# Kernel tuning notes

Measured on AMD Instinct MI355X. Metric: run time of the kernel, lower is better.

The kernel has to match this reference:

```python
import jax, jax.numpy as jnp
import numpy as np

N_NODES = 20000
N_EDGES = 640000
NODE_DIM = 128
EDGE_DIM = 128
HIDDEN = max(NODE_DIM, EDGE_DIM)  # 128


def _linear_init(key, fan_in, fan_out):
    # torch nn.Linear default: U(-1/sqrt(fan_in), 1/sqrt(fan_in))
    kw, kb = jax.random.split(key)
    bound = 1.0 / np.sqrt(fan_in)
    W = jax.random.uniform(kw, (fan_in, fan_out), jnp.float32, -bound, bound)
    b = jax.random.uniform(kb, (fan_out,), jnp.float32, -bound, bound)
    return W, b


def setup_inputs() -> dict:
    key = jax.random.key(0)
    ks = jax.random.split(key, 8)
    node_feat = jax.random.normal(ks[0], (N_NODES, NODE_DIM), jnp.float32)
    edge_feat = jax.random.normal(ks[1], (N_EDGES, EDGE_DIM), jnp.float32)
    edge_index = jax.random.randint(ks[2], (2, N_EDGES), 0, N_NODES, jnp.int64)
    W1e, b1e = _linear_init(ks[3], 2 * NODE_DIM + EDGE_DIM, HIDDEN)
    W2e, b2e = _linear_init(ks[4], HIDDEN, EDGE_DIM)
    W1n, b1n = _linear_init(ks[5], NODE_DIM + EDGE_DIM, NODE_DIM)
    W2n, b2n = _linear_init(ks[6], NODE_DIM, NODE_DIM)
    return {
        "node_feat": node_feat, "edge_feat": edge_feat, "edge_index": edge_index,
        "W1e": W1e, "b1e": b1e, "W2e": W2e, "b2e": b2e,
        "W1n": W1n, "b1n": b1n, "W2n": W2n, "b2n": b2n,
    }


def reference(node_feat, edge_feat, edge_index, W1e, b1e, W2e, b2e, W1n, b1n, W2n, b2n):
    src, dst = edge_index[0], edge_index[1]
    n_nodes = node_feat.shape[0]

    # Edge update: gather endpoints, concat, MLP, residual.
    edge_input = jnp.concatenate([edge_feat, node_feat[src], node_feat[dst]], axis=-1)
    h = jax.nn.silu(edge_input @ W1e + b1e)
    edge_feat = edge_feat + (h @ W2e + b2e)

    # Mean aggregation of updated edge feats into dst nodes (clamped counts).
    agg = jax.ops.segment_sum(edge_feat, dst, num_segments=n_nodes)
    counts = jax.ops.segment_sum(jnp.ones((dst.shape[0],), edge_feat.dtype), dst,
                                 num_segments=n_nodes)
    agg = agg / jnp.maximum(counts, 1.0)[:, None]

    # Node update: concat, MLP, residual.
    node_input = jnp.concatenate([node_feat, agg], axis=-1)
    g = jax.nn.silu(node_input @ W1n + b1n)
    node_feat = node_feat + (g @ W2n + b2n)
    return (node_feat, edge_feat)
```

## Files before the change

kernel.cpp:

```cpp
#include <hip/hip_runtime.h>
#include <hip/hip_bf16.h>
#include <stdint.h>

#define N_NODES 20000
#define N_EDGES 640000
#define DIM 128
#define TPB 10
#define EDGE_GRID 500

using bf16x8 = __attribute__((ext_vector_type(8))) short;
using f32x4  = __attribute__((ext_vector_type(4))) float;

static __device__ __forceinline__ unsigned short f2bf(float f) {
    union { float f; unsigned int u; } v; v.f = f;
    unsigned int r = v.u + 0x7FFFu + ((v.u >> 16) & 1u);
    return (unsigned short)(r >> 16);
}

static __device__ __forceinline__ void glds16(const unsigned short* g, char* lds) {
    __builtin_amdgcn_global_load_lds(
        (const __attribute__((address_space(1))) unsigned int*)(const void*)g,
        (__attribute__((address_space(3))) unsigned int*)(void*)lds, 16, 0, 0);
}

static __device__ __forceinline__ void lds_fence() {
    __builtin_amdgcn_sched_barrier(0);
    asm volatile("s_waitcnt lgkmcnt(0)" ::: "memory");
    __builtin_amdgcn_sched_barrier(0);
}
static __device__ __forceinline__ void ds_order() {
    __builtin_amdgcn_sched_barrier(0x7F);
}

__global__ void prep_kernel(const float* __restrict__ node_feat,
                            const float* __restrict__ W1e, const float* __restrict__ W2e,
                            const float* __restrict__ W1n, const float* __restrict__ W2n,
                            unsigned short* __restrict__ node_bf,
                            unsigned short* __restrict__ Wt1e, unsigned short* __restrict__ Wt2e,
                            unsigned short* __restrict__ Wt1n, unsigned short* __restrict__ Wt2n,
                            int* __restrict__ counts) {
    int tid = blockIdx.x * blockDim.x + threadIdx.x;
    int stride = gridDim.x * blockDim.x;
    for (int i = tid; i < N_NODES * DIM / 8; i += stride) {
        const float* p = node_feat + (size_t)i * 8;
        float4 f0 = *(const float4*)p;
        float4 f1 = *(const float4*)(p + 4);
        bf16x8 a;
        a[0] = (short)f2bf(f0.x); a[1] = (short)f2bf(f0.y);
        a[2] = (short)f2bf(f0.z); a[3] = (short)f2bf(f0.w);
        a[4] = (short)f2bf(f1.x); a[5] = (short)f2bf(f1.y);
        a[6] = (short)f2bf(f1.z); a[7] = (short)f2bf(f1.w);
        *(bf16x8*)(node_bf + (size_t)i * 8) = a;
    }
    for (int i = tid; i < DIM * 384; i += stride) { int n = i / 384, k = i % 384; Wt1e[i] = f2bf(W1e[k * DIM + n]); }
    for (int i = tid; i < DIM * DIM; i += stride) { int n = i / DIM, k = i % DIM; Wt2e[i] = f2bf(W2e[k * DIM + n]); }
    for (int i = tid; i < DIM * 256; i += stride) { int n = i / 256, k = i % 256; Wt1n[i] = f2bf(W1n[k * DIM + n]); }
    for (int i = tid; i < DIM * DIM; i += stride) { int n = i / DIM, k = i % DIM; Wt2n[i] = f2bf(W2n[k * DIM + n]); }
    for (int i = tid; i < N_NODES; i += stride) counts[i] = 0;
}

__global__ void count_kernel(const int* __restrict__ eidx, int* __restrict__ counts) {
    int e = blockIdx.x * blockDim.x + threadIdx.x;
    if (e < N_EDGES) atomicAdd(&counts[eidx[N_EDGES + e]], 1);
}

__global__ void scan_kernel(const int* __restrict__ counts, int* __restrict__ offsets,
                            int* __restrict__ cursor) {
    __shared__ int wsum[16];
    const int CH = 20;
    int tid = threadIdx.x;
    int lane = tid & 63, wid = tid >> 6;
    int base = tid * CH;
    int s = 0;
    #pragma unroll
    for (int j = 0; j < CH; ++j) { int i = base + j; s += (i < N_NODES) ? counts[i] : 0; }
    int chunk = s;
    #pragma unroll
    for (int off = 1; off < 64; off <<= 1) { int t = __shfl_up(s, off, 64); if (lane >= off) s += t; }
    if (lane == 63) wsum[wid] = s;
    __syncthreads();
    if (tid == 0) {
        int run = 0;
        for (int w = 0; w < 16; ++w) { int t = wsum[w]; wsum[w] = run; run += t; }
    }
    __syncthreads();
    int run = wsum[wid] + s - chunk;
    for (int j = 0; j < CH; ++j) {
        int i = base + j;
        if (i < N_NODES) { offsets[i] = run; cursor[i] = run; run += counts[i]; }
    }
}

__global__ void scatter_kernel(const int* __restrict__ eidx, int* __restrict__ cursor,
                               int* __restrict__ elist) {
    int e = blockIdx.x * blockDim.x + threadIdx.x;
    if (e < N_EDGES) {
        int p = atomicAdd(&cursor[eidx[N_EDGES + e]], 1);
        elist[p] = e;
    }
}

__launch_bounds__(256, 1)
__global__ void edge_kernel(const float* __restrict__ edge_feat,
                            const int* __restrict__ eidx,
                            const unsigned short* __restrict__ node_bf,
                            const unsigned short* __restrict__ Wt1e,
                            const unsigned short* __restrict__ Wt2e,
                            const float* __restrict__ b1e,
                            const float* __restrict__ b2e,
                            float* __restrict__ out_edge) {
    __shared__ char ldsW1[98304];
    __shared__ char ldsW2[32768];
    __shared__ char ldsS[4][4096];
    const int tid = threadIdx.x;
    const int wv = tid >> 6;
    const int l = tid & 63;
    const int lr = l & 15;
    const int kg = l >> 4;
    char* S = ldsS[wv];
    const int eBase = blockIdx.x * (TPB * 128);

    #pragma unroll
    for (int c = 0; c < 24; ++c) {
        int Sc = c * 256 + tid;
        int n = Sc / 48, sp = Sc % 48;
        int s = (sp & 56) | ((sp ^ n) & 7);
        glds16(Wt1e + n * 384 + s * 8, ldsW1 + Sc * 16);
    }
    #pragma unroll
    for (int c = 0; c < 8; ++c) {
        int Sc = c * 256 + tid;
        int n = Sc >> 4, sp = Sc & 15;
        int s = (sp & 8) | ((sp ^ n) & 7);
        glds16(Wt2e + n * 128 + s * 8, ldsW2 + Sc * 16);
    }

    float b1r[8], b2r[8];
    #pragma unroll
    for (int tt = 0; tt < 8; ++tt) { b1r[tt] = b1e[tt * 16 + lr]; b2r[tt] = b2e[tt * 16 + lr]; }

    float4 E0[4][2][2], E1[4][2][2];
    bf16x8 N0[8][2], N1[8][2];

    auto prefRaw = [&](int t, float4 (&E)[4][2][2], bf16x8 (&NB)[8][2]) {
        int tb = eBase + t * 128 + wv * 32;
        int e0 = tb + lr, e1 = tb + 16 + lr;
        int s0 = eidx[e0], d0 = eidx[N_EDGES + e0];
        int s1 = eidx[e1], d1 = eidx[N_EDGES + e1];
        #pragma unroll
        for (int st = 0; st < 4; ++st) {
            const float* p0 = edge_feat + (long)e0 * DIM + st * 32 + kg * 8;
            const float* p1 = edge_feat + (long)e1 * DIM + st * 32 + kg * 8;
            E[st][0][0] = *(const float4*)p0; E[st][0][1] = *(const float4*)(p0 + 4);
            E[st][1][0] = *(const float4*)p1; E[st][1][1] = *(const float4*)(p1 + 4);
        }
        #pragma unroll
        for (int st = 0; st < 4; ++st) {
            NB[st][0]     = *(const bf16x8*)(node_bf + (long)s0 * DIM + st * 32 + kg * 8);
            NB[st][1]     = *(const bf16x8*)(node_bf + (long)s1 * DIM + st * 32 + kg * 8);
            NB[st + 4][0] = *(const bf16x8*)(node_bf + (long)d0 * DIM + st * 32 + kg * 8);
            NB[st + 4][1] = *(const bf16x8*)(node_bf + (long)d1 * DIM + st * 32 + kg * 8);
        }
    };

    f32x4 acc[2][8];

    auto gemm1 = [&](float4 (&E)[4][2][2], bf16x8 (&NB)[8][2]) {
        bf16x8 EB[4][2];
        #pragma unroll
        for (int st = 0; st < 4; ++st)
            #pragma unroll
            for (int rt = 0; rt < 2; ++rt) {
                bf16x8 a;
                a[0] = (short)f2bf(E[st][rt][0].x); a[1] = (short)f2bf(E[st][rt][0].y);
                a[2] = (short)f2bf(E[st][rt][0].z); a[3] = (short)f2bf(E[st][rt][0].w);
                a[4] = (short)f2bf(E[st][rt][1].x); a[5] = (short)f2bf(E[st][rt][1].y);
                a[6] = (short)f2bf(E[st][rt][1].z); a[7] = (short)f2bf(E[st][rt][1].w);
                EB[st][rt] = a;
            }
        #pragma unroll
        for (int rt = 0; rt < 2; ++rt)
            #pragma unroll
            for (int tt = 0; tt < 8; ++tt) acc[rt][tt] = (f32x4){0.f, 0.f, 0.f, 0.f};
        #pragma unroll
        for (int s = 0; s < 12; ++s) {
            int sl = s * 4 + kg;
            int sp = (sl & 56) | ((sl ^ lr) & 7);
            #pragma unroll
            for (int tt = 0; tt < 8; ++tt) {
                bf16x8 B = *(const bf16x8*)(ldsW1 + (tt * 16 + lr) * 768 + sp * 16);
                #pragma unroll
                for (int rt = 0; rt < 2; ++rt) {
                    bf16x8 A = (s < 4) ? EB[s][rt] : NB[s - 4][rt];
                    acc[rt][tt] = __builtin_amdgcn_mfma_f32_16x16x32_bf16(A, B, acc[rt][tt], 0, 0, 0);
                }
            }
        }
    };

    auto tail = [&](int t) {
        int tb = eBase + t * 128 + wv * 32;
        f32x4 acc2[2][8];
        #pragma unroll
        for (int rt = 0; rt < 2; ++rt)
            #pragma unroll
            for (int tt = 0; tt < 8; ++tt) acc2[rt][tt] = (f32x4){0.f, 0.f, 0.f, 0.f};

        #pragma unroll
        for (int q = 0; q < 4; ++q) {
            #pragma unroll
            for (int rt = 0; rt < 2; ++rt)
                #pragma unroll
                for (int t2 = 0; t2 < 2; ++t2) {
                    int tt = q * 2 + t2;
                    #pragma unroll
                    for (int r = 0; r < 4; ++r) {
                        int row = rt * 16 + kg * 4 + r;
                        float x = acc[rt][tt][r] + b1r[tt];
                        float h = x / (1.0f + __expf(-x));
                        int slot = t2 * 2 + (lr >> 3);
                        int byte = row * 64 + ((slot ^ ((row >> 1) & 3)) << 4) + (lr & 7) * 2;
                        *(unsigned short*)(S + byte) = f2bf(h);
                    }
                }
            lds_fence();
            bf16x8 A2[2];
            #pragma unroll
            for (int rt = 0; rt < 2; ++rt) {
                int row = rt * 16 + lr;
                int byte = row * 64 + ((kg ^ ((row >> 1) & 3)) << 4);
                A2[rt] = *(const bf16x8*)(S + byte);
            }
            ds_order();
            int sl2 = q * 4 + kg;
            int sp2 = (sl2 & 8) | ((sl2 ^ lr) & 7);
            #pragma unroll
            for (int tt = 0; tt < 8; ++tt) {
                bf16x8 B = *(const bf16x8*)(ldsW2 + (tt * 16 + lr) * 256 + sp2 * 16);
                #pragma unroll
                for (int rt = 0; rt < 2; ++rt)
                    acc2[rt][tt] = __builtin_amdgcn_mfma_f32_16x16x32_bf16(A2[rt], B, acc2[rt][tt], 0, 0, 0);
            }
        }

        #pragma unroll
        for (int rt = 0; rt < 2; ++rt)
            #pragma unroll
            for (int ch = 0; ch < 2; ++ch) {
                #pragma unroll
                for (int t2 = 0; t2 < 4; ++t2) {
                    int tt = ch * 4 + t2;
                    #pragma unroll
                    for (int r = 0; r < 4; ++r) {
                        int row = kg * 4 + r;
                        int col = t2 * 16 + lr;
                        int byte = row * 256 + (((col >> 2) ^ (row & 15)) << 4) + (col & 3) * 4;
                        *(float*)(S + byte) = acc2[rt][tt][r] + b2r[tt];
                    }
                }
                lds_fence();
                #pragma unroll
                for (int i = 0; i < 4; ++i) {
                    int row = (l >> 4) + i * 4;
                    int slot = l & 15;
                    int byte = row * 256 + ((slot ^ (row & 15)) << 4);
                    float4 v = *(const float4*)(S + byte);
                    long gidx = (long)(tb + rt * 16 + row) * DIM + ch * 64 + slot * 4;
                    float4 rs = *(const float4*)(edge_feat + gidx);
                    v.x += rs.x; v.y += rs.y; v.z += rs.z; v.w += rs.w;
                    *(float4*)(out_edge + gidx) = v;
                }
                ds_order();
            }
    };

    prefRaw(0, E0, N0);
    __syncthreads();

    #pragma unroll 1
    for (int it = 0; it < TPB / 2; ++it) {
        int t0 = it * 2;
        prefRaw(t0 + 1, E1, N1);
        gemm1(E0, N0);
        tail(t0);
        if (t0 + 2 < TPB) prefRaw(t0 + 2, E0, N0);
        gemm1(E1, N1);
        tail(t0 + 1);
    }
}

__global__ void agg_kernel(const float* __restrict__ edge_out,
                           const int* __restrict__ offsets, const int* __restrict__ counts,
                           const int* __restrict__ elist,
                           unsigned short* __restrict__ agg_bf) {
    int n = blockIdx.x * 4 + (threadIdx.x >> 6);
    int l = threadIdx.x & 63;
    if (n >= N_NODES) return;
    int off = offsets[n], cnt = counts[n];
    float a0 = 0.f, a1 = 0.f;
    int i = 0;
    for (; i + 4 <= cnt; i += 4) {
        int e0 = elist[off + i], e1 = elist[off + i + 1];
        int e2 = elist[off + i + 2], e3 = elist[off + i + 3];
        float2 v0 = *(const float2*)(edge_out + (long)e0 * DIM + l * 2);
        float2 v1 = *(const float2*)(edge_out + (long)e1 * DIM + l * 2);
        float2 v2 = *(const float2*)(edge_out + (long)e2 * DIM + l * 2);
        float2 v3 = *(const float2*)(edge_out + (long)e3 * DIM + l * 2);
        a0 += v0.x + v1.x + v2.x + v3.x;
        a1 += v0.y + v1.y + v2.y + v3.y;
    }
    for (; i < cnt; ++i) {
        int e = elist[off + i];
        float2 v = *(const float2*)(edge_out + (long)e * DIM + l * 2);
        a0 += v.x; a1 += v.y;
    }
    float inv = 1.0f / fmaxf((float)cnt, 1.0f);
    agg_bf[n * DIM + l * 2] = f2bf(a0 * inv);
    agg_bf[n * DIM + l * 2 + 1] = f2bf(a1 * inv);
}

#define SLICE_B 8448
__launch_bounds__(256, 4)
__global__ void node_kernel(const float* __restrict__ node_feat,
                            const unsigned short* __restrict__ node_bf,
                            const unsigned short* __restrict__ agg_bf,
                            const unsigned short* __restrict__ Wt1n,
                            const unsigned short* __restrict__ Wt2n,
                            const float* __restrict__ b1n,
                            const float* __restrict__ b2n,
                            float* __restrict__ out_node) {
    __shared__ char lds[4][SLICE_B];
    const int tid = threadIdx.x;
    const int wv = tid >> 6;
    const int l = tid & 63;
    const int lr = l & 15;
    const int kg = l >> 4;
    char* slice = lds[wv];

    const int nBase = blockIdx.x * 128;
    const int wBase = nBase + wv * 32;

    int rowc[2];
    #pragma unroll
    for (int rt = 0; rt < 2; ++rt) {
        int row = wBase + rt * 16 + lr;
        rowc[rt] = row < N_NODES ? row : N_NODES - 1;
    }

    f32x4 acc[2][8];
    #pragma unroll
    for (int rt = 0; rt < 2; ++rt)
        #pragma unroll
        for (int t = 0; t < 8; ++t) acc[rt][t] = (f32x4){0.f, 0.f, 0.f, 0.f};

    #pragma unroll
    for (int s = 0; s < 8; ++s) {
        const int kk = s * 32 + kg * 8;
        bf16x8 A[2];
        if (s < 4) {
            #pragma unroll
            for (int rt = 0; rt < 2; ++rt)
                A[rt] = *(const bf16x8*)(node_bf + (long)rowc[rt] * DIM + kk);
        } else {
            #pragma unroll
            for (int rt = 0; rt < 2; ++rt)
                A[rt] = *(const bf16x8*)(agg_bf + (long)rowc[rt] * DIM + (kk - 128));
        }
        #pragma unroll
        for (int t = 0; t < 8; ++t) {
            bf16x8 B = *(const bf16x8*)(Wt1n + (t * 16 + lr) * 256 + kk);
            #pragma unroll
            for (int rt = 0; rt < 2; ++rt)
                acc[rt][t] = __builtin_amdgcn_mfma_f32_16x16x32_bf16(A[rt], B, acc[rt][t], 0, 0, 0);
        }
    }

    #pragma unroll
    for (int rt = 0; rt < 2; ++rt) {
        #pragma unroll
        for (int t = 0; t < 8; ++t) {
            float b1 = b1n[t * 16 + lr];
            int col = t * 16 + lr;
            #pragma unroll
            for (int r = 0; r < 4; ++r) {
                int row = rt * 16 + kg * 4 + r;
                float x = acc[rt][t][r] + b1;
                float h = x / (1.0f + __expf(-x));
                int byte = (row * 256 + col * 2) ^ ((row & 7) << 4);
                *(unsigned short*)(slice + byte) = f2bf(h);
            }
        }
    }
    __syncthreads();

    f32x4 acc2[2][8];
    #pragma unroll
    for (int rt = 0; rt < 2; ++rt)
        #pragma unroll
        for (int t = 0; t < 8; ++t) acc2[rt][t] = (f32x4){0.f, 0.f, 0.f, 0.f};

    #pragma unroll
    for (int s = 0; s < 4; ++s) {
        const int kk = s * 32 + kg * 8;
        bf16x8 A[2];
        #pragma unroll
        for (int rt = 0; rt < 2; ++rt) {
            int row = rt * 16 + lr;
            int byte = (row * 256 + kk * 2) ^ ((row & 7) << 4);
            A[rt] = *(const bf16x8*)(slice + byte);
        }
        #pragma unroll
        for (int t = 0; t < 8; ++t) {
            bf16x8 B = *(const bf16x8*)(Wt2n + (t * 16 + lr) * DIM + kk);
            #pragma unroll
            for (int rt = 0; rt < 2; ++rt)
                acc2[rt][t] = __builtin_amdgcn_mfma_f32_16x16x32_bf16(A[rt], B, acc2[rt][t], 0, 0, 0);
        }
    }
    __syncthreads();

    #pragma unroll
    for (int rt = 0; rt < 2; ++rt) {
        float* sf = (float*)slice;
        #pragma unroll
        for (int t = 0; t < 8; ++t) {
            float b2 = b2n[t * 16 + lr];
            int col = t * 16 + lr;
            #pragma unroll
            for (int r = 0; r < 4; ++r) {
                int row = kg * 4 + r;
                int colp = col ^ (row & 12);
                sf[row * 132 + colp] = acc2[rt][t][r] + b2;
            }
        }
        __syncthreads();
        #pragma unroll
        for (int rr = 0; rr < 8; ++rr) {
            int row = rr * 2 + (l >> 5);
            int c4 = (l & 31) * 4;
            int cswz = c4 ^ (row & 12);
            float4 v = *(const float4*)(sf + row * 132 + cswz);
            int grow = wBase + rt * 16 + row;
            if (grow < N_NODES) {
                long gidx = (long)grow * DIM + c4;
                float4 rsd = *(const float4*)(node_feat + gidx);
                v.x += rsd.x; v.y += rsd.y; v.z += rsd.z; v.w += rsd.w;
                *(float4*)(out_node + gidx) = v;
            }
        }
        __syncthreads();
    }
}

extern "C" void kernel_launch(void* const* d_in, const int* in_sizes, int n_in,
                              void* d_out, int out_size, void* d_ws, size_t ws_size,
                              hipStream_t stream) {
    const float* node_feat = (const float*)d_in[0];
    const float* edge_feat = (const float*)d_in[1];
    const int*   eidx      = (const int*)d_in[2];
    const float* W1e = (const float*)d_in[3];
    const float* b1e = (const float*)d_in[4];
    const float* W2e = (const float*)d_in[5];
    const float* b2e = (const float*)d_in[6];
    const float* W1n = (const float*)d_in[7];
    const float* b1n = (const float*)d_in[8];
    const float* W2n = (const float*)d_in[9];
    const float* b2n = (const float*)d_in[10];

    char* ws = (char*)d_ws;
    size_t off = 0;
    auto alloc = [&](size_t bytes) {
        void* p = ws + off;
        off += (bytes + 255) & ~(size_t)255;
        return p;
    };
    unsigned short* node_bf = (unsigned short*)alloc((size_t)N_NODES * DIM * 2);
    unsigned short* agg_bf  = (unsigned short*)alloc((size_t)N_NODES * DIM * 2);
    unsigned short* Wt1e    = (unsigned short*)alloc((size_t)DIM * 384 * 2);
    unsigned short* Wt2e    = (unsigned short*)alloc((size_t)DIM * DIM * 2);
    unsigned short* Wt1n    = (unsigned short*)alloc((size_t)DIM * 256 * 2);
    unsigned short* Wt2n    = (unsigned short*)alloc((size_t)DIM * DIM * 2);
    int* counts  = (int*)alloc((size_t)N_NODES * 4);
    int* offsets = (int*)alloc((size_t)N_NODES * 4);
    int* cursor  = (int*)alloc((size_t)N_NODES * 4);
    int* elist   = (int*)alloc((size_t)N_EDGES * 4);

    float* out_node = (float*)d_out;
    float* out_edge = out_node + (size_t)N_NODES * DIM;

    prep_kernel<<<512, 256, 0, stream>>>(node_feat, W1e, W2e, W1n, W2n,
                                         node_bf, Wt1e, Wt2e, Wt1n, Wt2n, counts);
    count_kernel<<<(N_EDGES + 255) / 256, 256, 0, stream>>>(eidx, counts);
    scan_kernel<<<1, 1024, 0, stream>>>(counts, offsets, cursor);
    scatter_kernel<<<(N_EDGES + 255) / 256, 256, 0, stream>>>(eidx, cursor, elist);
    edge_kernel<<<EDGE_GRID, 256, 0, stream>>>(edge_feat, eidx, node_bf, Wt1e, Wt2e,
                                               b1e, b2e, out_edge);
    agg_kernel<<<(N_NODES + 3) / 4, 256, 0, stream>>>(out_edge, offsets, counts, elist, agg_bf);
    node_kernel<<<(N_NODES + 127) / 128, 256, 0, stream>>>(node_feat, node_bf, agg_bf,
                                                           Wt1n, Wt2n, b1n, b2n, out_node);
}
```

Baseline: 518.8 us.

## Double edge-kernel block to 8 waves, single-buffer prefetch, preload residuals

The edge kernel goes from 4 to 8 waves per block (512 threads, launch bounds 512,2). Each block still covers the same 1280 edges in 5 tiles of 256. The explicit double-buffered register prefetch is replaced by a single buffer refilled after each tile, leaving latency hiding to the extra waves. Residual edge_feat rows are loaded ahead of the second GEMM, and the aggregation loop is widened to issue 8 gathers per step. This trades register-level software pipelining for more wave-level parallelism, with the risk of register-pressure spills under the new launch bounds and LDS limits on occupancy.

```diff
diff --git a/kernel.cpp b/kernel.cpp
--- a/kernel.cpp
+++ b/kernel.cpp
@@ -5,7 +5,7 @@
 #define N_NODES 20000
 #define N_EDGES 640000
 #define DIM 128
-#define TPB 10
+#define TPB 5
 #define EDGE_GRID 500
 
 using bf16x8 = __attribute__((ext_vector_type(8))) short;
@@ -30,6 +30,9 @@
 }
 static __device__ __forceinline__ void ds_order() {
     __builtin_amdgcn_sched_barrier(0x7F);
+}
+static __device__ __forceinline__ void vmem_order() {
+    __builtin_amdgcn_sched_barrier(0x38F);
 }
 
 __global__ void prep_kernel(const float* __restrict__ node_feat,
@@ -100,7 +103,7 @@
     }
 }
 
-__launch_bounds__(256, 1)
+__launch_bounds__(512, 2)
 __global__ void edge_kernel(const float* __restrict__ edge_feat,
                             const int* __restrict__ eidx,
                             const unsigned short* __restrict__ node_bf,
@@ -111,25 +114,25 @@
                             float* __restrict__ out_edge) {
     __shared__ char ldsW1[98304];
     __shared__ char ldsW2[32768];
-    __shared__ char ldsS[4][4096];
+    __shared__ char ldsS[8][4096];
     const int tid = threadIdx.x;
     const int wv = tid >> 6;
     const int l = tid & 63;
     const int lr = l & 15;
     const int kg = l >> 4;
     char* S = ldsS[wv];
-    const int eBase = blockIdx.x * (TPB * 128);
-
-    #pragma unroll
-    for (int c = 0; c < 24; ++c) {
-        int Sc = c * 256 + tid;
+    const int eBase = blockIdx.x * (TPB * 256);
+
+    #pragma unroll
+    for (int c = 0; c < 12; ++c) {
+        int Sc = c * 512 + tid;
         int n = Sc / 48, sp = Sc % 48;
         int s = (sp & 56) | ((sp ^ n) & 7);
         glds16(Wt1e + n * 384 + s * 8, ldsW1 + Sc * 16);
     }
     #pragma unroll
-    for (int c = 0; c < 8; ++c) {
-        int Sc = c * 256 + tid;
+    for (int c = 0; c < 4; ++c) {
+        int Sc = c * 512 + tid;
         int n = Sc >> 4, sp = Sc & 15;
         int s = (sp & 8) | ((sp ^ n) & 7);
         glds16(Wt2e + n * 128 + s * 8, ldsW2 + Sc * 16);
@@ -139,11 +142,11 @@
     #pragma unroll
     for (int tt = 0; tt < 8; ++tt) { b1r[tt] = b1e[tt * 16 + lr]; b2r[tt] = b2e[tt * 16 + lr]; }
 
-    float4 E0[4][2][2], E1[4][2][2];
-    bf16x8 N0[8][2], N1[8][2];
-
-    auto prefRaw = [&](int t, float4 (&E)[4][2][2], bf16x8 (&NB)[8][2]) {
-        int tb = eBase + t * 128 + wv * 32;
+    float4 E[4][2][2];
+    bf16x8 N[8][2];
+
+    auto prefRaw = [&](int t) {
+        int tb = eBase + t * 256 + wv * 32;
         int e0 = tb + lr, e1 = tb + 16 + lr;
         int s0 = eidx[e0], d0 = eidx[N_EDGES + e0];
         int s1 = eidx[e1], d1 = eidx[N_EDGES + e1];
@@ -156,16 +159,16 @@
         }
         #pragma unroll
         for (int st = 0; st < 4; ++st) {
-            NB[st][0]     = *(const bf16x8*)(node_bf + (long)s0 * DIM + st * 32 + kg * 8);
-            NB[st][1]     = *(const bf16x8*)(node_bf + (long)s1 * DIM + st * 32 + kg * 8);
-            NB[st + 4][0] = *(const bf16x8*)(node_bf + (long)d0 * DIM + st * 32 + kg * 8);
-            NB[st + 4][1] = *(const bf16x8*)(node_bf + (long)d1 * DIM + st * 32 + kg * 8);
+            N[st][0]     = *(const bf16x8*)(node_bf + (long)s0 * DIM + st * 32 + kg * 8);
+            N[st][1]     = *(const bf16x8*)(node_bf + (long)s1 * DIM + st * 32 + kg * 8);
+            N[st + 4][0] = *(const bf16x8*)(node_bf + (long)d0 * DIM + st * 32 + kg * 8);
+            N[st + 4][1] = *(const bf16x8*)(node_bf + (long)d1 * DIM + st * 32 + kg * 8);
         }
     };
 
     f32x4 acc[2][8];
 
-    auto gemm1 = [&](float4 (&E)[4][2][2], bf16x8 (&NB)[8][2]) {
+    auto gemm1 = [&]() {
         bf16x8 EB[4][2];
         #pragma unroll
         for (int st = 0; st < 4; ++st)
@@ -191,7 +194,7 @@
                 bf16x8 B = *(const bf16x8*)(ldsW1 + (tt * 16 + lr) * 768 + sp * 16);
                 #pragma unroll
                 for (int rt = 0; rt < 2; ++rt) {
-                    bf16x8 A = (s < 4) ? EB[s][rt] : NB[s - 4][rt];
+                    bf16x8 A = (s < 4) ? EB[s][rt] : N[s - 4][rt];
                     acc[rt][tt] = __builtin_amdgcn_mfma_f32_16x16x32_bf16(A, B, acc[rt][tt], 0, 0, 0);
                 }
             }
@@ -199,7 +202,22 @@
     };
 
     auto tail = [&](int t) {
-        int tb = eBase + t * 128 + wv * 32;
+        int tb = eBase + t * 256 + wv * 32;
+
+        float4 res[2][2][4];
+        #pragma unroll
+        for (int rt = 0; rt < 2; ++rt)
+            #pragma unroll
+            for (int ch = 0; ch < 2; ++ch)
+                #pragma unroll
+                for (int i = 0; i < 4; ++i) {
+                    int row = (l >> 4) + i * 4;
+                    int slot = l & 15;
+                    long gidx = (long)(tb + rt * 16 + row) * DIM + ch * 64 + slot * 4;
+                    res[rt][ch][i] = *(const float4*)(edge_feat + gidx);
+                }
+        vmem_order();
+
         f32x4 acc2[2][8];
         #pragma unroll
         for (int rt = 0; rt < 2; ++rt)
@@ -266,7 +284,7 @@
                     int byte = row * 256 + ((slot ^ (row & 15)) << 4);
                     float4 v = *(const float4*)(S + byte);
                     long gidx = (long)(tb + rt * 16 + row) * DIM + ch * 64 + slot * 4;
-                    float4 rs = *(const float4*)(edge_feat + gidx);
+                    float4 rs = res[rt][ch][i];
                     v.x += rs.x; v.y += rs.y; v.z += rs.z; v.w += rs.w;
                     *(float4*)(out_edge + gidx) = v;
                 }
@@ -274,18 +292,15 @@
             }
     };
 
-    prefRaw(0, E0, N0);
+    prefRaw(0);
     __syncthreads();
 
     #pragma unroll 1
-    for (int it = 0; it < TPB / 2; ++it) {
-        int t0 = it * 2;
-        prefRaw(t0 + 1, E1, N1);
-        gemm1(E0, N0);
-        tail(t0);
-        if (t0 + 2 < TPB) prefRaw(t0 + 2, E0, N0);
-        gemm1(E1, N1);
-        tail(t0 + 1);
+    for (int t = 0; t < TPB; ++t) {
+        gemm1();
+        tail(t);
+        vmem_order();
+        if (t + 1 < TPB) prefRaw(t + 1);
     }
 }
 
@@ -299,15 +314,15 @@
     int off = offsets[n], cnt = counts[n];
     float a0 = 0.f, a1 = 0.f;
     int i = 0;
-    for (; i + 4 <= cnt; i += 4) {
-        int e0 = elist[off + i], e1 = elist[off + i + 1];
-        int e2 = elist[off + i + 2], e3 = elist[off + i + 3];
-        float2 v0 = *(const float2*)(edge_out + (long)e0 * DIM + l * 2);
-        float2 v1 = *(const float2*)(edge_out + (long)e1 * DIM + l * 2);
-        float2 v2 = *(const float2*)(edge_out + (long)e2 * DIM + l * 2);
-        float2 v3 = *(const float2*)(edge_out + (long)e3 * DIM + l * 2);
-        a0 += v0.x + v1.x + v2.x + v3.x;
-        a1 += v0.y + v1.y + v2.y + v3.y;
+    for (; i + 8 <= cnt; i += 8) {
+        int ee[8];
+        #pragma unroll
+        for (int j = 0; j < 8; ++j) ee[j] = elist[off + i + j];
+        float2 vv[8];
+        #pragma unroll
+        for (int j = 0; j < 8; ++j) vv[j] = *(const float2*)(edge_out + (long)ee[j] * DIM + l * 2);
+        #pragma unroll
+        for (int j = 0; j < 8; ++j) { a0 += vv[j].x; a1 += vv[j].y; }
     }
     for (; i < cnt; ++i) {
         int e = elist[off + i];
@@ -493,7 +508,7 @@
     count_kernel<<<(N_EDGES + 255) / 256, 256, 0, stream>>>(eidx, counts);
     scan_kernel<<<1, 1024, 0, stream>>>(counts, offsets, cursor);
     scatter_kernel<<<(N_EDGES + 255) / 256, 256, 0, stream>>>(eidx, cursor, elist);
-    edge_kernel<<<EDGE_GRID, 256, 0, stream>>>(edge_feat, eidx, node_bf, Wt1e, Wt2e,
+    edge_kernel<<<EDGE_GRID, 512, 0, stream>>>(edge_feat, eidx, node_bf, Wt1e, Wt2e,
                                                b1e, b2e, out_edge);
     agg_kernel<<<(N_NODES + 3) / 4, 256, 0, stream>>>(out_edge, offsets, counts, elist, agg_bf);
     node_kernel<<<(N_NODES + 127) / 128, 256, 0, stream>>>(node_feat, node_bf, agg_bf,
```

Measured after the change: 660.7 us. +27.4%, slower.
